# Optimization experiments

Measured on AMD Instinct MI355X. Metric: run time of the kernel, lower is better.

The kernel has to match this reference:

```python
import jax, jax.numpy as jnp
import numpy as np

EPS = 1e-5
K = 9
DILATION = 1

def bn(x, g, b, m, v):
    # x: (B,C,N,1), inference-mode BatchNorm2d with running stats
    sh = (1, -1, 1, 1)
    return (x - m.reshape(sh)) * (g.reshape(sh) / jnp.sqrt(v.reshape(sh) + EPS)) + b.reshape(sh)

def conv1x1(x, w, b):
    # w: (Cout, Cin), x: (B,Cin,N,1)
    return jnp.einsum('oc,bcnj->bonj', w, x) + b.reshape(1, -1, 1, 1)

def knn_idx(feat, k):
    # feat: (B,C,N) -> (B,N,k) indices of k nearest nodes (incl. self)
    xt = jnp.transpose(feat, (0, 2, 1))  # (B,N,C)
    x2 = jnp.sum(xt * xt, axis=-1)       # (B,N)
    dist = x2[:, :, None] - 2.0 * jnp.einsum('bnc,bmc->bnm', xt, xt) + x2[:, None, :]
    _, idx = jax.lax.top_k(-dist, k)
    return idx

def setup_inputs():
    key = jax.random.key(0)
    ks = jax.random.split(key, 24)
    B, C, H, W = 16, 256, 32, 32
    HID = 512
    def g(i, shape, s=1.0):
        return jax.random.normal(ks[i], shape, dtype=jnp.float32) * s
    def pos(i, shape):
        return jax.random.uniform(ks[i], shape, dtype=jnp.float32, minval=0.5, maxval=1.5)
    return {
        'x': g(0, (B, C, H, W)),
        'fc1_w': g(1, (C, C), 0.05), 'fc1_b': g(2, (C,), 0.05),
        'bn1_g': pos(3, (C,)), 'bn1_b': g(4, (C,), 0.1), 'bn1_m': g(5, (C,), 0.1), 'bn1_v': pos(6, (C,)),
        'gc_w': g(7, (HID, 2 * C), 0.05), 'gc_b': g(8, (HID,), 0.05),
        'gbn_g': pos(9, (HID,)), 'gbn_b': g(10, (HID,), 0.1), 'gbn_m': g(11, (HID,), 0.1), 'gbn_v': pos(12, (HID,)),
        'bn2_g': pos(13, (HID,)), 'bn2_b': g(14, (HID,), 0.1), 'bn2_m': g(15, (HID,), 0.1), 'bn2_v': pos(16, (HID,)),
        'fc2_w': g(17, (C, HID), 0.05), 'fc2_b': g(18, (C,), 0.05),
        'bn3_g': pos(19, (C,)), 'bn3_b': g(20, (C,), 0.1), 'bn3_m': g(21, (C,), 0.1), 'bn3_v': pos(22, (C,)),
    }

def reference(x, fc1_w, fc1_b, bn1_g, bn1_b, bn1_m, bn1_v,
              gc_w, gc_b, gbn_g, gbn_b, gbn_m, gbn_v,
              bn2_g, bn2_b, bn2_m, bn2_v,
              fc2_w, fc2_b, bn3_g, bn3_b, bn3_m, bn3_v):
    B, C, H, W = x.shape
    N = H * W
    x = x.reshape(B, C, N, 1)
    shortcut = x
    # fc1: 1x1 conv + BN
    h = bn(conv1x1(x, fc1_w, fc1_b), bn1_g, bn1_b, bn1_m, bn1_v)
    # DyGraphConv2d: dynamic dilated kNN graph over N nodes
    feat = h[..., 0]  # (B,C,N)
    idx = knn_idx(feat, K * DILATION)[:, :, ::DILATION]  # (B,N,K)
    # MRConv2d: max over neighbors of (x_j - x_i)
    x_j = jax.vmap(lambda f, i: f[:, i])(feat, idx)        # (B,C,N,K) gather
    diff_max = jnp.max(x_j - feat[:, :, :, None], axis=-1)  # (B,C,N)
    # interleave [x, max_diff] along channel dim -> (B, 2C, N, 1)
    m = jnp.stack([feat, diff_max], axis=2).reshape(B, 2 * C, N, 1)
    g = conv1x1(m, gc_w, gc_b)
    g = bn(g, gbn_g, gbn_b, gbn_m, gbn_v)  # BasicConv BN, act='None'
    # graph_conv Sequential: BN + GELU (erf, torch default)
    g = jax.nn.gelu(bn(g, bn2_g, bn2_b, bn2_m, bn2_v), approximate=False)
    # fc2 + residual (drop_path=0 -> identity)
    out = bn(conv1x1(g, fc2_w, fc2_b), bn3_g, bn3_b, bn3_m, bn3_v)
    return out + shortcut
```

## Files before the change

### kernel.cpp

```cpp
#include <hip/hip_runtime.h>
#include <hip/hip_bf16.h>
#include <stdint.h>

typedef unsigned long long u64;
typedef __hip_bfloat16 bf16;
typedef short s8v __attribute__((ext_vector_type(8)));
typedef short s4v __attribute__((ext_vector_type(4)));
typedef float f4v __attribute__((ext_vector_type(4)));

#define B_   16
#define C_   256
#define N_   1024
#define HID_ 512

#define GLD16(g, l)                                                         \
    __builtin_amdgcn_global_load_lds(                                       \
        (const __attribute__((address_space(1))) void*)(g),                 \
        (__attribute__((address_space(3))) void*)(l), 16, 0, 0)

__device__ __forceinline__ unsigned short f2b(float f) {
    unsigned u = __float_as_uint(f);
    unsigned r = (u + 0x7FFFu + ((u >> 16) & 1u)) >> 16;
    return (unsigned short)r;
}
__device__ __forceinline__ float b2f(unsigned short s) {
    return __uint_as_float(((unsigned)s) << 16);
}
__device__ __forceinline__ float ldIn(const void* p, long long i, int bf) {
    return bf ? b2f(((const unsigned short*)p)[i]) : ((const float*)p)[i];
}
__device__ __forceinline__ u64 shfl_xor_u64(u64 v, int m) {
    unsigned lo = (unsigned)v, hi = (unsigned)(v >> 32);
    lo = __shfl_xor(lo, m, 64);
    hi = __shfl_xor(hi, m, 64);
    return ((u64)hi << 32) | lo;
}

__global__ void prep_kernel(const void* xp,
    const void* fc1_b, const void* bn1_g, const void* bn1_b, const void* bn1_m, const void* bn1_v,
    const void* gc_b,  const void* gbn_g, const void* gbn_b, const void* gbn_m, const void* gbn_v,
    const void* bn2_g, const void* bn2_b, const void* bn2_m, const void* bn2_v,
    const void* fc2_b, const void* bn3_g, const void* bn3_b, const void* bn3_m, const void* bn3_v,
    int* flags, float* s1, float* t1, float* Sg, float* Tg, float* s3, float* t3,
    float* x2)
{
    __shared__ int sf;
    if (threadIdx.x == 0) {
        const unsigned short* u = (const unsigned short*)xp;
        int cnt = 0;
        for (int i = 0; i < 64; ++i) {
            int e = (u[2 * i] >> 7) & 0xFF;
            cnt += (e >= 87 && e <= 167);
        }
        int f = (cnt >= 48) ? 1 : 0;
        flags[0] = f;
        sf = f;
    }
    for (int i = threadIdx.x; i < B_ * N_; i += 512) x2[i] = 0.f;
    __syncthreads();
    int bf = sf;
    int i = threadIdx.x;
    if (i < 256) {
        float g = ldIn(bn1_g, i, bf), bb = ldIn(bn1_b, i, bf);
        float m = ldIn(bn1_m, i, bf), v  = ldIn(bn1_v, i, bf);
        float s = g / sqrtf(v + 1e-5f);
        s1[i] = s;
        t1[i] = (ldIn(fc1_b, i, bf) - m) * s + bb;

        float g3 = ldIn(bn3_g, i, bf), b3 = ldIn(bn3_b, i, bf);
        float m3 = ldIn(bn3_m, i, bf), v3 = ldIn(bn3_v, i, bf);
        float ss3 = g3 / sqrtf(v3 + 1e-5f);
        s3[i] = ss3;
        t3[i] = (ldIn(fc2_b, i, bf) - m3) * ss3 + b3;
    }
    if (i < 512) {
        float gg = ldIn(gbn_g, i, bf), gb = ldIn(gbn_b, i, bf);
        float gm = ldIn(gbn_m, i, bf), gv = ldIn(gbn_v, i, bf);
        float sg = gg / sqrtf(gv + 1e-5f);
        float g2 = ldIn(bn2_g, i, bf), b2 = ldIn(bn2_b, i, bf);
        float m2 = ldIn(bn2_m, i, bf), v2 = ldIn(bn2_v, i, bf);
        float s2 = g2 / sqrtf(v2 + 1e-5f);
        Sg[i] = sg * s2;
        Tg[i] = ((ldIn(gc_b, i, bf) - gm) * sg + gb - m2) * s2 + b2;
    }
}

__global__ __launch_bounds__(256)
void cast_weights(const void* w1, const void* wg, const void* w2,
                  short* W1h, short* W1l, short* Wgb, short* W2b,
                  const int* flags)
{
    int inf = flags[0];
    int i = blockIdx.x * 256 + threadIdx.x;
    if (i < 65536) {
        float f = ldIn(w1, i, inf);
        unsigned short h = f2b(f);
        W1h[i] = (short)h;
        W1l[i] = (short)f2b(f - b2f(h));
    } else if (i < 65536 + 262144) {
        int j = i - 65536;
        Wgb[j] = (short)f2b(ldIn(wg, j, inf));
    } else {
        int j = i - 327680;
        W2b[j] = (short)f2b(ldIn(w2, j, inf));
    }
}

__global__ __launch_bounds__(256)
void transpose_split_x(const void* __restrict__ X, short* __restrict__ xth,
                       short* __restrict__ xtl, const int* __restrict__ flags)
{
    __shared__ float tile[64][68];
    int inf = flags[0];
    int t = threadIdx.x;
    int n0 = blockIdx.x * 64, c0 = blockIdx.y * 64, b = blockIdx.z;

    #pragma unroll
    for (int rr = 0; rr < 4; ++rr) {
        int cl = (t >> 4) + rr * 16;
        int nl = (t & 15) * 4;
        long long g = ((long long)b * C_ + c0 + cl) * N_ + n0 + nl;
        if (inf) {
            s4v v = *(const s4v*)((const short*)X + g);
            tile[cl][nl + 0] = b2f((unsigned short)v[0]);
            tile[cl][nl + 1] = b2f((unsigned short)v[1]);
            tile[cl][nl + 2] = b2f((unsigned short)v[2]);
            tile[cl][nl + 3] = b2f((unsigned short)v[3]);
        } else {
            f4v v = *(const f4v*)((const float*)X + g);
            tile[cl][nl + 0] = v[0]; tile[cl][nl + 1] = v[1];
            tile[cl][nl + 2] = v[2]; tile[cl][nl + 3] = v[3];
        }
    }
    __syncthreads();

    int nl = t >> 2, cseg = t & 3;
    long long base = ((long long)((b << 10) + n0 + nl)) * C_ + c0 + cseg * 16;
    s8v h0, h1, l0, l1;
    #pragma unroll
    for (int cc = 0; cc < 16; ++cc) {
        float f = tile[cseg * 16 + cc][nl];
        unsigned short h = f2b(f);
        unsigned short l = f2b(f - b2f(h));
        if (cc < 8) { h0[cc] = (short)h; l0[cc] = (short)l; }
        else        { h1[cc - 8] = (short)h; l1[cc - 8] = (short)l; }
    }
    *(s8v*)(xth + base)     = h0;
    *(s8v*)(xth + base + 8) = h1;
    *(s8v*)(xtl + base)     = l0;
    *(s8v*)(xtl + base + 8) = l1;
}

__global__ __launch_bounds__(256)
void fc1_mfma(const short* __restrict__ W1h, const short* __restrict__ W1l,
              const short* __restrict__ xth, const short* __restrict__ xtl,
              const float* __restrict__ s1, const float* __restrict__ t1,
              float* __restrict__ Ft, short* __restrict__ Fhi,
              short* __restrict__ Flo, float* __restrict__ x2)
{
    __shared__ __align__(16) char ldsbuf[32768];

    int t = threadIdx.x;
    int n0 = blockIdx.x * 64, o0 = blockIdx.y * 128, b = blockIdx.z;
    int wv = t >> 6, lane = t & 63, ln15 = t & 15, quad = (t >> 4) & 3;

    int csw = (((lane & 3) ^ ((lane >> 3) & 3))) * 8;
    const short* gAh = W1h + (long long)(o0 + wv * 32 + (lane >> 2)) * C_ + csw;
    const short* gAl = W1l + (long long)(o0 + wv * 32 + (lane >> 2)) * C_ + csw;
    short* lH0 = (short*)(ldsbuf)           + wv * 32 * 32;
    short* lL0 = (short*)(ldsbuf + 8192)    + wv * 32 * 32;
    short* lH1 = (short*)(ldsbuf + 16384)   + wv * 32 * 32;
    short* lL1 = (short*)(ldsbuf + 24576)   + wv * 32 * 32;

#define FC1_STAGE(kc_, bi_) do {                                              \
        short* dh = (bi_) ? lH1 : lH0;                                        \
        short* dl = (bi_) ? lL1 : lL0;                                        \
        GLD16(gAh + (kc_) * 32,            dh);                               \
        GLD16(gAh + (kc_) * 32 + 16 * C_,  dh + 16 * 32);                     \
        GLD16(gAl + (kc_) * 32,            dl);                               \
        GLD16(gAl + (kc_) * 32 + 16 * C_,  dl + 16 * 32);                     \
    } while (0)

    FC1_STAGE(0, 0);

    s8v xh[8], xl[8];
    {
        long long xoff = (long long)((b << 10) + n0 + wv * 16 + ln15) * C_ + quad * 8;
        #pragma unroll
        for (int kc = 0; kc < 8; ++kc) {
            xh[kc] = *(const s8v*)(xth + xoff + kc * 32);
            xl[kc] = *(const s8v*)(xtl + xoff + kc * 32);
        }
    }

    f4v acc[8];
    #pragma unroll
    for (int i = 0; i < 8; ++i) acc[i] = 0.f;

    int roff = (quad ^ ((ln15 >> 1) & 3)) * 8;

    __syncthreads();

    #pragma unroll
    for (int kc = 0; kc < 8; ++kc) {
        if (kc < 7) FC1_STAGE(kc + 1, (kc + 1) & 1);
        const short* Ah_c = (const short*)(ldsbuf + (kc & 1) * 16384);
        const short* Al_c = Ah_c + 4096;
        #pragma unroll
        for (int i = 0; i < 8; ++i) {
            s8v wh8 = *(const s8v*)&Ah_c[(i * 16 + ln15) * 32 + roff];
            s8v wl8 = *(const s8v*)&Al_c[(i * 16 + ln15) * 32 + roff];
            acc[i] = __builtin_amdgcn_mfma_f32_16x16x32_bf16(wh8, xh[kc], acc[i], 0, 0, 0);
            acc[i] = __builtin_amdgcn_mfma_f32_16x16x32_bf16(wh8, xl[kc], acc[i], 0, 0, 0);
            acc[i] = __builtin_amdgcn_mfma_f32_16x16x32_bf16(wl8, xh[kc], acc[i], 0, 0, 0);
        }
        __syncthreads();
    }
#undef FC1_STAGE

    int n = n0 + wv * 16 + ln15;
    long long nb = (long long)(b << 10) + n;
    float p2 = 0.f;
    #pragma unroll
    for (int i = 0; i < 8; ++i) {
        int ob = o0 + i * 16 + quad * 4;
        f4v f;
        s4v hi, lo;
        #pragma unroll
        for (int r = 0; r < 4; ++r) {
            float v = acc[i][r] * s1[ob + r] + t1[ob + r];
            f[r] = v;
            unsigned short h = f2b(v);
            hi[r] = (short)h;
            lo[r] = (short)f2b(v - b2f(h));
            p2 += v * v;
        }
        *(f4v*)(Ft  + nb * C_ + ob) = f;
        *(s4v*)(Fhi + nb * C_ + ob) = hi;
        *(s4v*)(Flo + nb * C_ + ob) = lo;
    }
    p2 += __shfl_xor(p2, 16, 64);
    p2 += __shfl_xor(p2, 32, 64);
    if (quad == 0) atomicAdd(&x2[nb], p2);
}

__global__ __launch_bounds__(256)
void gram_topk(const short* __restrict__ Fhi, const short* __restrict__ Flo,
               const float* __restrict__ x2, u64* __restrict__ Part)
{
    __shared__ __align__(16) char ldsbuf[32768];
    u64*   mrg  = (u64*)(ldsbuf);
    u64*   mrg2 = (u64*)(ldsbuf + 20480);

    int t = threadIdx.x;
    int q0 = blockIdx.x * 64, mq = blockIdx.y, b = blockIdx.z;
    int wv = t >> 6, lane = t & 63, ln15 = t & 15, quad = (t >> 4) & 3;

    int csw = (((lane & 3) ^ ((lane >> 3) & 3))) * 8;
    const short* gAh = Fhi + (long long)((b << 10) + mq * 128 + wv * 32 + (lane >> 2)) * C_ + csw;
    const short* gAl = Flo + (long long)((b << 10) + mq * 128 + wv * 32 + (lane >> 2)) * C_ + csw;
    short* lH0 = (short*)(ldsbuf)           + wv * 32 * 32;
    short* lL0 = (short*)(ldsbuf + 8192)    + wv * 32 * 32;
    short* lH1 = (short*)(ldsbuf + 16384)   + wv * 32 * 32;
    short* lL1 = (short*)(ldsbuf + 24576)   + wv * 32 * 32;

#define GRAM_STAGE(kc_, bi_) do {                                             \
        short* dh = (bi_) ? lH1 : lH0;                                        \
        short* dl = (bi_) ? lL1 : lL0;                                        \
        GLD16(gAh + (kc_) * 32,            dh);                               \
        GLD16(gAh + (kc_) * 32 + 16 * C_,  dh + 16 * 32);                     \
        GLD16(gAl + (kc_) * 32,            dl);                               \
        GLD16(gAl + (kc_) * 32 + 16 * C_,  dl + 16 * 32);                     \
    } while (0)

    GRAM_STAGE(0, 0);

    s8v qh[8], ql[8];
    {
        long long qoff = (long long)((b << 10) + q0 + wv * 16 + ln15) * C_ + quad * 8;
        #pragma unroll
        for (int kc = 0; kc < 8; ++kc) {
            qh[kc] = *(const s8v*)(Fhi + qoff + kc * 32);
            ql[kc] = *(const s8v*)(Flo + qoff + kc * 32);
        }
    }

    f4v acc[8];
    #pragma unroll
    for (int i = 0; i < 8; ++i) acc[i] = 0.f;

    int roff = (quad ^ ((ln15 >> 1) & 3)) * 8;

    __syncthreads();

    #pragma unroll
    for (int kc = 0; kc < 8; ++kc) {
        if (kc < 7) GRAM_STAGE(kc + 1, (kc + 1) & 1);
        const short* Ah_c = (const short*)(ldsbuf + (kc & 1) * 16384);
        const short* Al_c = Ah_c + 4096;
        #pragma unroll
        for (int i = 0; i < 8; ++i) {
            s8v mh = *(const s8v*)&Ah_c[(i * 16 + ln15) * 32 + roff];
            s8v ml = *(const s8v*)&Al_c[(i * 16 + ln15) * 32 + roff];
            acc[i] = __builtin_amdgcn_mfma_f32_16x16x32_bf16(mh, qh[kc], acc[i], 0, 0, 0);
            acc[i] = __builtin_amdgcn_mfma_f32_16x16x32_bf16(mh, ql[kc], acc[i], 0, 0, 0);
            acc[i] = __builtin_amdgcn_mfma_f32_16x16x32_bf16(ml, qh[kc], acc[i], 0, 0, 0);
        }
        __syncthreads();
    }
#undef GRAM_STAGE

    const float* x2p = x2 + (b << 10) + mq * 128 + quad * 4;

    u64 l[9];
    #pragma unroll
    for (int i = 0; i < 9; ++i) l[i] = ~0ULL;
    #pragma unroll
    for (int i = 0; i < 8; ++i) {
        f4v xv = *(const f4v*)(x2p + i * 16);
        #pragma unroll
        for (int r = 0; r < 4; ++r) {
            int mloc = i * 16 + quad * 4 + r;
            float d = xv[r] - 2.f * acc[i][r];
            unsigned u = __float_as_uint(d);
            u = (u & 0x80000000u) ? ~u : (u | 0x80000000u);
            u64 key = ((u64)u << 32) | (unsigned)(mq * 128 + mloc);
            if (key < l[8]) {
                u64 x = key;
                #pragma unroll
                for (int jj = 0; jj < 9; ++jj) {
                    u64 lo2 = l[jj] < x ? l[jj] : x;
                    u64 hi2 = l[jj] < x ? x : l[jj];
                    l[jj] = lo2; x = hi2;
                }
            }
        }
    }

    __syncthreads();
    {
        int qloc = wv * 16 + ln15;
        #pragma unroll
        for (int k = 0; k < 9; ++k) mrg[(qloc * 4 + quad) * 9 + k] = l[k];
    }
    __syncthreads();
    if (t < 128) {
        int r = t >> 1, pr = t & 1;
        const u64* LA = &mrg[(r * 4 + pr * 2) * 9];
        const u64* LB = LA + 9;
        int ia = 0, ib = 0;
        u64* Po = &mrg2[(r * 2 + pr) * 9];
        #pragma unroll
        for (int k = 0; k < 9; ++k) {
            u64 va = LA[ia], vb = LB[ib];
            bool ta = va < vb;
            Po[k] = ta ? va : vb;
            ia += ta; ib += !ta;
        }
    }
    __syncthreads();
    if (t < 64) {
        const u64* LA = &mrg2[(t * 2) * 9];
        const u64* LB = LA + 9;
        int ia = 0, ib = 0;
        u64* P = Part + (((long long)((b << 10) + q0 + t)) * 8 + mq) * 9;
        #pragma unroll
        for (int k = 0; k < 9; ++k) {
            u64 va = LA[ia], vb = LB[ib];
            bool ta = va < vb;
            P[k] = ta ? va : vb;
            ia += ta; ib += !ta;
        }
    }
}

__global__ __launch_bounds__(256)
void build_Mt(const float* __restrict__ Ft, const u64* __restrict__ Part,
              short* __restrict__ Mt)
{
    int t = threadIdx.x;
    int wv = t >> 6, lane = t & 63;
    int n = blockIdx.x * 4 + wv;
    int b = blockIdx.y;
    long long nb = (long long)(b << 10) + n;

    const u64* L = Part + nb * 72 + (long long)(lane & 7) * 9;
    u64 l[9];
    #pragma unroll
    for (int k = 0; k < 9; ++k) l[k] = L[k];
    #pragma unroll
    for (int s = 1; s <= 4; s <<= 1) {
        u64 p[9];
        #pragma unroll
        for (int k = 0; k < 9; ++k) p[k] = shfl_xor_u64(l[k], s);
        #pragma unroll
        for (int k = 0; k < 9; ++k) {
            u64 x = p[k];
            if (x < l[8]) {
                #pragma unroll
                for (int jj = 0; jj < 9; ++jj) {
                    u64 lo2 = l[jj] < x ? l[jj] : x;
                    u64 hi2 = l[jj] < x ? x : l[jj];
                    l[jj] = lo2; x = hi2;
                }
            }
        }
    }

    int c0 = lane * 4;
    f4v f = *(const f4v*)(Ft + nb * C_ + c0);
    f4v mx = {-3.4e38f, -3.4e38f, -3.4e38f, -3.4e38f};
    #pragma unroll
    for (int k = 0; k < 9; ++k) {
        int id = (int)(l[k] & 0xFFFFFFFFu);
        f4v g = *(const f4v*)(Ft + ((long long)(b << 10) + id) * C_ + c0);
        mx[0] = fmaxf(mx[0], g[0]); mx[1] = fmaxf(mx[1], g[1]);
        mx[2] = fmaxf(mx[2], g[2]); mx[3] = fmaxf(mx[3], g[3]);
    }
    s8v m8;
    #pragma unroll
    for (int r = 0; r < 4; ++r) {
        m8[2 * r]     = (short)f2b(f[r]);
        m8[2 * r + 1] = (short)f2b(mx[r] - f[r]);
    }
    *(s8v*)(Mt + nb * (2 * C_) + 2 * c0) = m8;
}

template<int EPI, int K_>
__global__ __launch_bounds__(256)
void mfma_gemm(const short* __restrict__ A, const short* __restrict__ Bm,
               void* __restrict__ Out, const float* __restrict__ scale,
               const float* __restrict__ bias, const void* __restrict__ resid,
               const int* __restrict__ flags, int Odim)
{
    __shared__ __align__(16) char ldsbuf[16384];

    int t = threadIdx.x, b = blockIdx.z;
    int n0 = blockIdx.x * 64, o0 = blockIdx.y * 128;
    int wv = t >> 6, lane = t & 63, ln15 = t & 15, quad = (t >> 4) & 3;

    int csw = (((lane & 3) ^ ((lane >> 3) & 3))) * 8;
    const short* gA = A + (long long)(o0 + wv * 32 + (lane >> 2)) * K_ + csw;
    short* l0 = (short*)(ldsbuf)        + wv * 32 * 32;
    short* l1 = (short*)(ldsbuf + 8192) + wv * 32 * 32;

#define GEMM_STAGE(kc_, bi_) do {                                             \
        short* d = (bi_) ? l1 : l0;                                           \
        GLD16(gA + (kc_) * 32,            d);                                 \
        GLD16(gA + (kc_) * 32 + 16 * K_,  d + 16 * 32);                       \
    } while (0)

    GEMM_STAGE(0, 0);

    constexpr int NKC = K_ / 32;
    s8v bfr[NKC];
    {
        long long boff = (long long)((b << 10) + n0 + wv * 16 + ln15) * K_ + quad * 8;
        #pragma unroll
        for (int kc = 0; kc < NKC; ++kc)
            bfr[kc] = *(const s8v*)(Bm + boff + kc * 32);
    }

    f4v acc[8];
    #pragma unroll
    for (int i = 0; i < 8; ++i) acc[i] = 0.f;

    int roff = (quad ^ ((ln15 >> 1) & 3)) * 8;

    __syncthreads();

    #pragma unroll
    for (int kc = 0; kc < NKC; ++kc) {
        if (kc < NKC - 1) GEMM_STAGE(kc + 1, (kc + 1) & 1);
        const short* Ac = (const short*)(ldsbuf + (kc & 1) * 8192);
        #pragma unroll
        for (int i = 0; i < 8; ++i) {
            s8v a = *(const s8v*)&Ac[(i * 16 + ln15) * 32 + roff];
            acc[i] = __builtin_amdgcn_mfma_f32_16x16x32_bf16(a, bfr[kc], acc[i], 0, 0, 0);
        }
        __syncthreads();
    }
#undef GEMM_STAGE

    int inf = flags[0];
    int n = n0 + wv * 16 + ln15;
    #pragma unroll
    for (int i = 0; i < 8; ++i) {
        int ob = o0 + i * 16 + quad * 4;
        if (EPI == 0) {
            s4v g;
            #pragma unroll
            for (int r = 0; r < 4; ++r) {
                float val = acc[i][r] * scale[ob + r] + bias[ob + r];
                val = 0.5f * val * (1.0f + erff(val * 0.70710678118654752f));
                g[r] = (short)f2b(val);
            }
            *(s4v*)((short*)Out + ((long long)((b << 10) + n)) * Odim + ob) = g;
        } else {
            #pragma unroll
            for (int r = 0; r < 4; ++r) {
                int o = ob + r;
                long long oi = ((long long)b * Odim + o) * N_ + n;
                ((float*)Out)[oi] = acc[i][r] * scale[o] + bias[o] + ldIn(resid, oi, inf);
            }
        }
    }
}

extern "C" void kernel_launch(void* const* d_in, const int* in_sizes, int n_in,
                              void* d_out, int out_size, void* d_ws, size_t ws_size,
                              hipStream_t stream)
{
    const void* p[23];
    if (n_in >= 23 && in_sizes[0] != 4194304 && in_sizes[22] == 4194304) {
        const int amap[23] = {
            22, 13, 12, 1, 0, 2, 3,
            21, 20, 17, 16, 18, 19,
            5, 4, 6, 7,
            15, 14, 9, 8, 10, 11 };
        for (int i = 0; i < 23; ++i) p[i] = d_in[amap[i]];
    } else {
        for (int i = 0; i < 23; ++i) p[i] = d_in[i];
    }

    const void* x     = p[0];
    const void* fc1_w = p[1];
    const void* fc1_b = p[2];
    const void* bn1_g = p[3];
    const void* bn1_b = p[4];
    const void* bn1_m = p[5];
    const void* bn1_v = p[6];
    const void* gc_w  = p[7];
    const void* gc_b  = p[8];
    const void* gbn_g = p[9];
    const void* gbn_b = p[10];
    const void* gbn_m = p[11];
    const void* gbn_v = p[12];
    const void* bn2_g = p[13];
    const void* bn2_b = p[14];
    const void* bn2_m = p[15];
    const void* bn2_v = p[16];
    const void* fc2_w = p[17];
    const void* fc2_b = p[18];
    const void* bn3_g = p[19];
    const void* bn3_b = p[20];
    const void* bn3_m = p[21];
    const void* bn3_v = p[22];

    char* ws = (char*)d_ws;
    size_t off = 0;
    int*   flags = (int*)ws;
    float* s1 = (float*)(ws + 256);
    float* t1 = s1 + 256;
    float* s3 = t1 + 256;
    float* t3 = s3 + 256;
    float* Sg = t3 + 256;
    float* Tg = Sg + 512;
    off = 16384;
    short* W1h   = (short*)(ws + off); off += (size_t)C_ * C_ * 2;
    short* W1l   = (short*)(ws + off); off += (size_t)C_ * C_ * 2;
    short* Wgb   = (short*)(ws + off); off += (size_t)HID_ * 2 * C_ * 2;
    short* W2b   = (short*)(ws + off); off += (size_t)C_ * HID_ * 2;
    short* xth   = (short*)(ws + off); off += (size_t)B_ * N_ * C_ * 2;
    short* xtl   = (short*)(ws + off); off += (size_t)B_ * N_ * C_ * 2;
    float* Ft    = (float*)(ws + off); off += (size_t)B_ * N_ * C_ * 4;
    short* Fhi   = (short*)(ws + off); off += (size_t)B_ * N_ * C_ * 2;
    short* Flo   = (short*)(ws + off); off += (size_t)B_ * N_ * C_ * 2;
    float* x2    = (float*)(ws + off); off += (size_t)B_ * N_ * 4;
    u64*   Part  = (u64*)  (ws + off); off += (size_t)B_ * N_ * 8 * 9 * 8;
    short* Mt    = (short*)(ws + off); off += (size_t)B_ * N_ * 2 * C_ * 2;
    short* Gt    = (short*)(ws + off); off += (size_t)B_ * N_ * HID_ * 2;

    prep_kernel<<<1, 512, 0, stream>>>(x,
        fc1_b, bn1_g, bn1_b, bn1_m, bn1_v,
        gc_b, gbn_g, gbn_b, gbn_m, gbn_v,
        bn2_g, bn2_b, bn2_m, bn2_v,
        fc2_b, bn3_g, bn3_b, bn3_m, bn3_v,
        flags, s1, t1, Sg, Tg, s3, t3, x2);

    cast_weights<<<1792, 256, 0, stream>>>(fc1_w, gc_w, fc2_w,
                                           W1h, W1l, Wgb, W2b, flags);

    transpose_split_x<<<dim3(16, 4, 16), 256, 0, stream>>>(x, xth, xtl, flags);

    fc1_mfma<<<dim3(16, 2, 16), 256, 0, stream>>>(
        W1h, W1l, xth, xtl, s1, t1, Ft, Fhi, Flo, x2);

    gram_topk<<<dim3(16, 8, 16), 256, 0, stream>>>(Fhi, Flo, x2, Part);

    build_Mt<<<dim3(256, 16), 256, 0, stream>>>(Ft, Part, Mt);

    mfma_gemm<0, 512><<<dim3(16, 4, 16), 256, 0, stream>>>(
        Wgb, Mt, Gt, Sg, Tg, nullptr, flags, HID_);

    mfma_gemm<1, 512><<<dim3(16, 2, 16), 256, 0, stream>>>(
        W2b, Gt, d_out, s3, t3, x, flags, C_);
}
```

Baseline: 294.8 us.

## Process two 128-candidate chunks per gram_topk block to halve partial lists

Result: slower. 363.7 us (+23.4%).

```diff
diff --git a/kernel.cpp b/kernel.cpp
--- a/kernel.cpp
+++ b/kernel.cpp
@@ -248,32 +248,35 @@
 void gram_topk(const short* __restrict__ Fhi, const short* __restrict__ Flo,
                const float* __restrict__ x2, u64* __restrict__ Part)
 {
-    __shared__ __align__(16) char ldsbuf[32768];
+    __shared__ __align__(16) char ldsbuf[33792];
+    float* x2s = (float*)(ldsbuf + 32768);
     u64*   mrg  = (u64*)(ldsbuf);
     u64*   mrg2 = (u64*)(ldsbuf + 20480);
 
     int t = threadIdx.x;
-    int q0 = blockIdx.x * 64, mq = blockIdx.y, b = blockIdx.z;
+    int q0 = blockIdx.x * 64, my = blockIdx.y, b = blockIdx.z;
     int wv = t >> 6, lane = t & 63, ln15 = t & 15, quad = (t >> 4) & 3;
 
     int csw = (((lane & 3) ^ ((lane >> 3) & 3))) * 8;
-    const short* gAh = Fhi + (long long)((b << 10) + mq * 128 + wv * 32 + (lane >> 2)) * C_ + csw;
-    const short* gAl = Flo + (long long)((b << 10) + mq * 128 + wv * 32 + (lane >> 2)) * C_ + csw;
+    const short* gAh = Fhi + (long long)((b << 10) + my * 256 + wv * 32 + (lane >> 2)) * C_ + csw;
+    const short* gAl = Flo + (long long)((b << 10) + my * 256 + wv * 32 + (lane >> 2)) * C_ + csw;
     short* lH0 = (short*)(ldsbuf)           + wv * 32 * 32;
     short* lL0 = (short*)(ldsbuf + 8192)    + wv * 32 * 32;
     short* lH1 = (short*)(ldsbuf + 16384)   + wv * 32 * 32;
     short* lL1 = (short*)(ldsbuf + 24576)   + wv * 32 * 32;
 
-#define GRAM_STAGE(kc_, bi_) do {                                             \
+#define GRAM_STAGE(c_, kc_, bi_) do {                                         \
         short* dh = (bi_) ? lH1 : lH0;                                        \
         short* dl = (bi_) ? lL1 : lL0;                                        \
-        GLD16(gAh + (kc_) * 32,            dh);                               \
-        GLD16(gAh + (kc_) * 32 + 16 * C_,  dh + 16 * 32);                     \
-        GLD16(gAl + (kc_) * 32,            dl);                               \
-        GLD16(gAl + (kc_) * 32 + 16 * C_,  dl + 16 * 32);                     \
+        GLD16(gAh + (c_) * 128 * C_ + (kc_) * 32,            dh);             \
+        GLD16(gAh + (c_) * 128 * C_ + (kc_) * 32 + 16 * C_,  dh + 16 * 32);   \
+        GLD16(gAl + (c_) * 128 * C_ + (kc_) * 32,            dl);             \
+        GLD16(gAl + (c_) * 128 * C_ + (kc_) * 32 + 16 * C_,  dl + 16 * 32);   \
     } while (0)
 
-    GRAM_STAGE(0, 0);
+    GRAM_STAGE(0, 0, 0);
+
+    x2s[t] = x2[(b << 10) + my * 256 + t];
 
     s8v qh[8], ql[8];
     {
@@ -291,51 +294,53 @@
 
     int roff = (quad ^ ((ln15 >> 1) & 3)) * 8;
 
-    __syncthreads();
-
-    #pragma unroll
-    for (int kc = 0; kc < 8; ++kc) {
-        if (kc < 7) GRAM_STAGE(kc + 1, (kc + 1) & 1);
-        const short* Ah_c = (const short*)(ldsbuf + (kc & 1) * 16384);
-        const short* Al_c = Ah_c + 4096;
+    u64 l[9];
+    #pragma unroll
+    for (int i = 0; i < 9; ++i) l[i] = ~0ULL;
+
+    __syncthreads();
+
+    #pragma unroll
+    for (int c = 0; c < 2; ++c) {
+        #pragma unroll
+        for (int kc = 0; kc < 8; ++kc) {
+            if (kc < 7)      GRAM_STAGE(c, kc + 1, (kc + 1) & 1);
+            else if (c == 0) GRAM_STAGE(1, 0, 0);
+            const short* Ah_c = (const short*)(ldsbuf + (kc & 1) * 16384);
+            const short* Al_c = Ah_c + 4096;
+            #pragma unroll
+            for (int i = 0; i < 8; ++i) {
+                s8v mh = *(const s8v*)&Ah_c[(i * 16 + ln15) * 32 + roff];
+                s8v ml = *(const s8v*)&Al_c[(i * 16 + ln15) * 32 + roff];
+                acc[i] = __builtin_amdgcn_mfma_f32_16x16x32_bf16(mh, qh[kc], acc[i], 0, 0, 0);
+                acc[i] = __builtin_amdgcn_mfma_f32_16x16x32_bf16(mh, ql[kc], acc[i], 0, 0, 0);
+                acc[i] = __builtin_amdgcn_mfma_f32_16x16x32_bf16(ml, qh[kc], acc[i], 0, 0, 0);
+            }
+            __syncthreads();
+        }
         #pragma unroll
         for (int i = 0; i < 8; ++i) {
-            s8v mh = *(const s8v*)&Ah_c[(i * 16 + ln15) * 32 + roff];
-            s8v ml = *(const s8v*)&Al_c[(i * 16 + ln15) * 32 + roff];
-            acc[i] = __builtin_amdgcn_mfma_f32_16x16x32_bf16(mh, qh[kc], acc[i], 0, 0, 0);
-            acc[i] = __builtin_amdgcn_mfma_f32_16x16x32_bf16(mh, ql[kc], acc[i], 0, 0, 0);
-            acc[i] = __builtin_amdgcn_mfma_f32_16x16x32_bf16(ml, qh[kc], acc[i], 0, 0, 0);
-        }
-        __syncthreads();
-    }
-#undef GRAM_STAGE
-
-    const float* x2p = x2 + (b << 10) + mq * 128 + quad * 4;
-
-    u64 l[9];
-    #pragma unroll
-    for (int i = 0; i < 9; ++i) l[i] = ~0ULL;
-    #pragma unroll
-    for (int i = 0; i < 8; ++i) {
-        f4v xv = *(const f4v*)(x2p + i * 16);
-        #pragma unroll
-        for (int r = 0; r < 4; ++r) {
-            int mloc = i * 16 + quad * 4 + r;
-            float d = xv[r] - 2.f * acc[i][r];
-            unsigned u = __float_as_uint(d);
-            u = (u & 0x80000000u) ? ~u : (u | 0x80000000u);
-            u64 key = ((u64)u << 32) | (unsigned)(mq * 128 + mloc);
-            if (key < l[8]) {
-                u64 x = key;
-                #pragma unroll
-                for (int jj = 0; jj < 9; ++jj) {
-                    u64 lo2 = l[jj] < x ? l[jj] : x;
-                    u64 hi2 = l[jj] < x ? x : l[jj];
-                    l[jj] = lo2; x = hi2;
+            #pragma unroll
+            for (int r = 0; r < 4; ++r) {
+                int mloc = i * 16 + quad * 4 + r;
+                float d = x2s[c * 128 + mloc] - 2.f * acc[i][r];
+                unsigned u = __float_as_uint(d);
+                u = (u & 0x80000000u) ? ~u : (u | 0x80000000u);
+                u64 key = ((u64)u << 32) | (unsigned)(my * 256 + c * 128 + mloc);
+                if (key < l[8]) {
+                    u64 x = key;
+                    #pragma unroll
+                    for (int jj = 0; jj < 9; ++jj) {
+                        u64 lo2 = l[jj] < x ? l[jj] : x;
+                        u64 hi2 = l[jj] < x ? x : l[jj];
+                        l[jj] = lo2; x = hi2;
+                    }
                 }
             }
-        }
-    }
+            acc[i] = 0.f;
+        }
+    }
+#undef GRAM_STAGE
 
     __syncthreads();
     {
@@ -363,7 +368,7 @@
         const u64* LA = &mrg2[(t * 2) * 9];
         const u64* LB = LA + 9;
         int ia = 0, ib = 0;
-        u64* P = Part + (((long long)((b << 10) + q0 + t)) * 8 + mq) * 9;
+        u64* P = Part + (((long long)((b << 10) + q0 + t)) * 4 + my) * 9;
         #pragma unroll
         for (int k = 0; k < 9; ++k) {
             u64 va = LA[ia], vb = LB[ib];
@@ -384,12 +389,12 @@
     int b = blockIdx.y;
     long long nb = (long long)(b << 10) + n;
 
-    const u64* L = Part + nb * 72 + (long long)(lane & 7) * 9;
+    const u64* L = Part + nb * 36 + (long long)(lane & 3) * 9;
     u64 l[9];
     #pragma unroll
     for (int k = 0; k < 9; ++k) l[k] = L[k];
     #pragma unroll
-    for (int s = 1; s <= 4; s <<= 1) {
+    for (int s = 1; s <= 2; s <<= 1) {
         u64 p[9];
         #pragma unroll
         for (int k = 0; k < 9; ++k) p[k] = shfl_xor_u64(l[k], s);
@@ -586,7 +591,7 @@
     fc1_mfma<<<dim3(16, 2, 16), 256, 0, stream>>>(
         W1h, W1l, xth, xtl, s1, t1, Ft, Fhi, Flo, x2);
 
-    gram_topk<<<dim3(16, 8, 16), 256, 0, stream>>>(Fhi, Flo, x2, Part);
+    gram_topk<<<dim3(16, 4, 16), 256, 0, stream>>>(Fhi, Flo, x2, Part);
 
     build_Mt<<<dim3(256, 16), 256, 0, stream>>>(Ft, Part, Mt);
 
```

## Triple-buffer LDS staging with single barrier per k-step in GEMM kernels

Applied to the files above, without the earlier changes.

Result: faster. 284.2 us (-3.6%).

```diff
diff --git a/kernel.cpp b/kernel.cpp
--- a/kernel.cpp
+++ b/kernel.cpp
@@ -17,6 +17,22 @@
     __builtin_amdgcn_global_load_lds(                                       \
         (const __attribute__((address_space(1))) void*)(g),                 \
         (__attribute__((address_space(3))) void*)(l), 16, 0, 0)
+
+#define WAITB4() do {                                                       \
+        asm volatile("s_waitcnt vmcnt(4)" ::: "memory");                    \
+        __builtin_amdgcn_s_barrier();                                       \
+        __builtin_amdgcn_sched_barrier(0);                                  \
+    } while (0)
+#define WAITB2() do {                                                       \
+        asm volatile("s_waitcnt vmcnt(2)" ::: "memory");                    \
+        __builtin_amdgcn_s_barrier();                                       \
+        __builtin_amdgcn_sched_barrier(0);                                  \
+    } while (0)
+#define WAITB0() do {                                                       \
+        asm volatile("s_waitcnt vmcnt(0)" ::: "memory");                    \
+        __builtin_amdgcn_s_barrier();                                       \
+        __builtin_amdgcn_sched_barrier(0);                                  \
+    } while (0)
 
 __device__ __forceinline__ unsigned short f2b(float f) {
     unsigned u = __float_as_uint(f);
@@ -158,7 +174,7 @@
               float* __restrict__ Ft, short* __restrict__ Fhi,
               short* __restrict__ Flo, float* __restrict__ x2)
 {
-    __shared__ __align__(16) char ldsbuf[32768];
+    __shared__ __align__(16) char ldsbuf[49152];
 
     int t = threadIdx.x;
     int n0 = blockIdx.x * 64, o0 = blockIdx.y * 128, b = blockIdx.z;
@@ -167,21 +183,19 @@
     int csw = (((lane & 3) ^ ((lane >> 3) & 3))) * 8;
     const short* gAh = W1h + (long long)(o0 + wv * 32 + (lane >> 2)) * C_ + csw;
     const short* gAl = W1l + (long long)(o0 + wv * 32 + (lane >> 2)) * C_ + csw;
-    short* lH0 = (short*)(ldsbuf)           + wv * 32 * 32;
-    short* lL0 = (short*)(ldsbuf + 8192)    + wv * 32 * 32;
-    short* lH1 = (short*)(ldsbuf + 16384)   + wv * 32 * 32;
-    short* lL1 = (short*)(ldsbuf + 24576)   + wv * 32 * 32;
-
-#define FC1_STAGE(kc_, bi_) do {                                              \
-        short* dh = (bi_) ? lH1 : lH0;                                        \
-        short* dl = (bi_) ? lL1 : lL0;                                        \
+    int slotofs = wv * 32 * 32;
+
+#define FC1_STAGE(kc_) do {                                                   \
+        short* base_ = (short*)(ldsbuf + ((kc_) % 3) * 16384);                \
+        short* dh = base_ + slotofs;                                          \
+        short* dl = base_ + 4096 + slotofs;                                   \
         GLD16(gAh + (kc_) * 32,            dh);                               \
         GLD16(gAh + (kc_) * 32 + 16 * C_,  dh + 16 * 32);                     \
         GLD16(gAl + (kc_) * 32,            dl);                               \
         GLD16(gAl + (kc_) * 32 + 16 * C_,  dl + 16 * 32);                     \
     } while (0)
 
-    FC1_STAGE(0, 0);
+    FC1_STAGE(0);
 
     s8v xh[8], xl[8];
     {
@@ -193,18 +207,19 @@
         }
     }
 
+    FC1_STAGE(1);
+
     f4v acc[8];
     #pragma unroll
     for (int i = 0; i < 8; ++i) acc[i] = 0.f;
 
     int roff = (quad ^ ((ln15 >> 1) & 3)) * 8;
 
-    __syncthreads();
-
     #pragma unroll
     for (int kc = 0; kc < 8; ++kc) {
-        if (kc < 7) FC1_STAGE(kc + 1, (kc + 1) & 1);
-        const short* Ah_c = (const short*)(ldsbuf + (kc & 1) * 16384);
+        if (kc < 7) WAITB4(); else WAITB0();
+        if (kc < 6) FC1_STAGE(kc + 2);
+        const short* Ah_c = (const short*)(ldsbuf + (kc % 3) * 16384);
         const short* Al_c = Ah_c + 4096;
         #pragma unroll
         for (int i = 0; i < 8; ++i) {
@@ -214,7 +229,6 @@
             acc[i] = __builtin_amdgcn_mfma_f32_16x16x32_bf16(wh8, xl[kc], acc[i], 0, 0, 0);
             acc[i] = __builtin_amdgcn_mfma_f32_16x16x32_bf16(wl8, xh[kc], acc[i], 0, 0, 0);
         }
-        __syncthreads();
     }
 #undef FC1_STAGE
 
@@ -248,7 +262,8 @@
 void gram_topk(const short* __restrict__ Fhi, const short* __restrict__ Flo,
                const float* __restrict__ x2, u64* __restrict__ Part)
 {
-    __shared__ __align__(16) char ldsbuf[32768];
+    __shared__ __align__(16) char ldsbuf[49664];
+    float* x2s = (float*)(ldsbuf + 49152);
     u64*   mrg  = (u64*)(ldsbuf);
     u64*   mrg2 = (u64*)(ldsbuf + 20480);
 
@@ -259,21 +274,21 @@
     int csw = (((lane & 3) ^ ((lane >> 3) & 3))) * 8;
     const short* gAh = Fhi + (long long)((b << 10) + mq * 128 + wv * 32 + (lane >> 2)) * C_ + csw;
     const short* gAl = Flo + (long long)((b << 10) + mq * 128 + wv * 32 + (lane >> 2)) * C_ + csw;
-    short* lH0 = (short*)(ldsbuf)           + wv * 32 * 32;
-    short* lL0 = (short*)(ldsbuf + 8192)    + wv * 32 * 32;
-    short* lH1 = (short*)(ldsbuf + 16384)   + wv * 32 * 32;
-    short* lL1 = (short*)(ldsbuf + 24576)   + wv * 32 * 32;
-
-#define GRAM_STAGE(kc_, bi_) do {                                             \
-        short* dh = (bi_) ? lH1 : lH0;                                        \
-        short* dl = (bi_) ? lL1 : lL0;                                        \
+    int slotofs = wv * 32 * 32;
+
+#define GRAM_STAGE(kc_) do {                                                  \
+        short* base_ = (short*)(ldsbuf + ((kc_) % 3) * 16384);                \
+        short* dh = base_ + slotofs;                                          \
+        short* dl = base_ + 4096 + slotofs;                                   \
         GLD16(gAh + (kc_) * 32,            dh);                               \
         GLD16(gAh + (kc_) * 32 + 16 * C_,  dh + 16 * 32);                     \
         GLD16(gAl + (kc_) * 32,            dl);                               \
         GLD16(gAl + (kc_) * 32 + 16 * C_,  dl + 16 * 32);                     \
     } while (0)
 
-    GRAM_STAGE(0, 0);
+    GRAM_STAGE(0);
+
+    if (t < 128) x2s[t] = x2[(b << 10) + mq * 128 + t];
 
     s8v qh[8], ql[8];
     {
@@ -285,18 +300,19 @@
         }
     }
 
+    GRAM_STAGE(1);
+
     f4v acc[8];
     #pragma unroll
     for (int i = 0; i < 8; ++i) acc[i] = 0.f;
 
     int roff = (quad ^ ((ln15 >> 1) & 3)) * 8;
 
-    __syncthreads();
-
     #pragma unroll
     for (int kc = 0; kc < 8; ++kc) {
-        if (kc < 7) GRAM_STAGE(kc + 1, (kc + 1) & 1);
-        const short* Ah_c = (const short*)(ldsbuf + (kc & 1) * 16384);
+        if (kc < 7) WAITB4(); else WAITB0();
+        if (kc < 6) GRAM_STAGE(kc + 2);
+        const short* Ah_c = (const short*)(ldsbuf + (kc % 3) * 16384);
         const short* Al_c = Ah_c + 4096;
         #pragma unroll
         for (int i = 0; i < 8; ++i) {
@@ -306,22 +322,18 @@
             acc[i] = __builtin_amdgcn_mfma_f32_16x16x32_bf16(mh, ql[kc], acc[i], 0, 0, 0);
             acc[i] = __builtin_amdgcn_mfma_f32_16x16x32_bf16(ml, qh[kc], acc[i], 0, 0, 0);
         }
-        __syncthreads();
     }
 #undef GRAM_STAGE
 
-    const float* x2p = x2 + (b << 10) + mq * 128 + quad * 4;
-
     u64 l[9];
     #pragma unroll
     for (int i = 0; i < 9; ++i) l[i] = ~0ULL;
     #pragma unroll
     for (int i = 0; i < 8; ++i) {
-        f4v xv = *(const f4v*)(x2p + i * 16);
         #pragma unroll
         for (int r = 0; r < 4; ++r) {
             int mloc = i * 16 + quad * 4 + r;
-            float d = xv[r] - 2.f * acc[i][r];
+            float d = x2s[mloc] - 2.f * acc[i][r];
             unsigned u = __float_as_uint(d);
             u = (u & 0x80000000u) ? ~u : (u | 0x80000000u);
             u64 key = ((u64)u << 32) | (unsigned)(mq * 128 + mloc);
@@ -433,7 +445,7 @@
                const float* __restrict__ bias, const void* __restrict__ resid,
                const int* __restrict__ flags, int Odim)
 {
-    __shared__ __align__(16) char ldsbuf[16384];
+    __shared__ __align__(16) char ldsbuf[24576];
 
     int t = threadIdx.x, b = blockIdx.z;
     int n0 = blockIdx.x * 64, o0 = blockIdx.y * 128;
@@ -441,16 +453,15 @@
 
     int csw = (((lane & 3) ^ ((lane >> 3) & 3))) * 8;
     const short* gA = A + (long long)(o0 + wv * 32 + (lane >> 2)) * K_ + csw;
-    short* l0 = (short*)(ldsbuf)        + wv * 32 * 32;
-    short* l1 = (short*)(ldsbuf + 8192) + wv * 32 * 32;
-
-#define GEMM_STAGE(kc_, bi_) do {                                             \
-        short* d = (bi_) ? l1 : l0;                                           \
+    int slotofs = wv * 32 * 32;
+
+#define GEMM_STAGE(kc_) do {                                                  \
+        short* d = (short*)(ldsbuf + ((kc_) % 3) * 8192) + slotofs;           \
         GLD16(gA + (kc_) * 32,            d);                                 \
         GLD16(gA + (kc_) * 32 + 16 * K_,  d + 16 * 32);                       \
     } while (0)
 
-    GEMM_STAGE(0, 0);
+    GEMM_STAGE(0);
 
     constexpr int NKC = K_ / 32;
     s8v bfr[NKC];
@@ -461,24 +472,24 @@
             bfr[kc] = *(const s8v*)(Bm + boff + kc * 32);
     }
 
+    GEMM_STAGE(1);
+
     f4v acc[8];
     #pragma unroll
     for (int i = 0; i < 8; ++i) acc[i] = 0.f;
 
     int roff = (quad ^ ((ln15 >> 1) & 3)) * 8;
 
-    __syncthreads();
-
     #pragma unroll
     for (int kc = 0; kc < NKC; ++kc) {
-        if (kc < NKC - 1) GEMM_STAGE(kc + 1, (kc + 1) & 1);
-        const short* Ac = (const short*)(ldsbuf + (kc & 1) * 8192);
+        if (kc < NKC - 1) WAITB2(); else WAITB0();
+        if (kc < NKC - 2) GEMM_STAGE(kc + 2);
+        const short* Ac = (const short*)(ldsbuf + (kc % 3) * 8192);
         #pragma unroll
         for (int i = 0; i < 8; ++i) {
             s8v a = *(const s8v*)&Ac[(i * 16 + ln15) * 32 + roff];
             acc[i] = __builtin_amdgcn_mfma_f32_16x16x32_bf16(a, bfr[kc], acc[i], 0, 0, 0);
         }
-        __syncthreads();
     }
 #undef GEMM_STAGE
 
```
